# Kernel optimization log

Measured on AMD Instinct MI355X. Metric: run time of the kernel, lower is better.

The kernel has to match this reference:

```python
import jax, jax.numpy as jnp
import numpy as np

G, T, H, E, F, C = 8, 2048, 512, 8, 2048, 256


def setup_inputs() -> dict:
    key = jax.random.key(0)
    ks = jax.random.split(key, 4)
    s = 0.02  # truncated-normal stddev in the original init (plain normal here)
    return {
        "x": jax.random.normal(ks[0], (G, T, H), jnp.float32),
        "router_kernel": jax.random.normal(ks[1], (H, E), jnp.float32) * s,
        "router_bias": jnp.zeros((E,), jnp.float32),
        "wi": jax.random.normal(ks[2], (E, H, F), jnp.float32) * s,
        "bi": jnp.zeros((E, F), jnp.float32),
        "wo": jax.random.normal(ks[3], (E, F, H), jnp.float32) * s,
        "bo": jnp.zeros((E, H), jnp.float32),
        "expert_capacity": C,
    }


def reference(x, router_kernel, router_bias, wi, bi, wo, bo, expert_capacity):
    # ---- Router (eval mode: no jitter noise, no dropout) ----
    # logits / probs: [g, t, e]
    router_logits = jnp.einsum("gth,he->gte", x, router_kernel) + router_bias
    router_probs = jax.nn.softmax(router_logits, axis=-1)

    # Experts-choose masked routing: each expert picks its top-capacity tokens.
    probs_et = jnp.swapaxes(router_probs, 1, 2)              # [g, e, t]
    expert_gate, expert_index = jax.lax.top_k(probs_et, expert_capacity)  # [g, e, c]
    dispatch = jax.nn.one_hot(expert_index, x.shape[1], dtype=x.dtype)    # [g, e, c, t]
    combine = dispatch * expert_gate[..., None]                            # [g, e, c, t]

    # ---- Dispatch: gather tokens into per-expert buffers ----
    expert_inputs = jnp.einsum("gect,gth->gech", dispatch, x)  # [g, e, c, h]

    # ---- Per-expert FFN (batched einsum GEMMs) ----
    h_mid = jax.nn.gelu(
        jnp.einsum("gech,ehf->gecf", expert_inputs, wi) + bi[None, :, None, :],
        approximate=False,
    )
    expert_out = jnp.einsum("gecf,efh->gech", h_mid, wo) + bo[None, :, None, :]

    # ---- Combine: scatter expert outputs back, scaled by router prob ----
    y = jnp.einsum("gect,gech->gth", combine, expert_out)  # [g, t, h]
    return y
```

## Files before the change

### kernel.cpp

```cpp
#include <hip/hip_runtime.h>
#include <cstdint>
#include <cstddef>

#define G_ 8
#define T_ 2048
#define H_ 512
#define E_ 8
#define F_ 2048
#define C_ 256

typedef __bf16 bf16x8 __attribute__((ext_vector_type(8)));
typedef float f32x4 __attribute__((ext_vector_type(4)));

__device__ __forceinline__ unsigned short f2bf(float f) {
  unsigned u = __float_as_uint(f);
  u += 0x7FFFu + ((u >> 16) & 1u);
  return (unsigned short)(u >> 16);
}

__device__ __forceinline__ void gload_lds16(const void* g, void* l) {
  __builtin_amdgcn_global_load_lds(
      (const __attribute__((address_space(1))) void*)g,
      (__attribute__((address_space(3))) void*)l, 16, 0, 0);
}

__device__ __forceinline__ float fast_gelu(float v) {
  float z = v * (1.5957691216f + 0.0713540727f * v * v);
  float e = __expf(-z);
  return v * __builtin_amdgcn_rcpf(1.0f + e);
}

#define BARRIER() do { __builtin_amdgcn_s_barrier(); asm volatile("" ::: "memory"); } while (0)
#define WAIT_LDS() do { asm volatile("s_waitcnt lgkmcnt(0)" ::: "memory"); \
                        __builtin_amdgcn_sched_barrier(0); } while (0)

__device__ __forceinline__ void transconv_body(const float* __restrict__ in,
                                               unsigned short* __restrict__ out,
                                               int R, int Cc, int tC, int bidrem,
                                               float* smem) {
  int tid = threadIdx.x;
  int nT = (R / 64) * tC;
  int b = bidrem / nT;
  int rem = bidrem % nT;
  int tr = rem / tC, tc = rem % tC;
  const float* ib = in + (size_t)b * R * Cc + (size_t)(tr * 64) * Cc + tc * 64;
  unsigned short* ob = out + (size_t)b * R * Cc;
  int lr = tid >> 4, lc = (tid & 15) * 4;
#pragma unroll
  for (int i = 0; i < 4; ++i) {
    float4 v = *(const float4*)&ib[(size_t)(lr + 16 * i) * Cc + lc];
    smem[(lr + 16 * i) * 65 + lc + 0] = v.x;
    smem[(lr + 16 * i) * 65 + lc + 1] = v.y;
    smem[(lr + 16 * i) * 65 + lc + 2] = v.z;
    smem[(lr + 16 * i) * 65 + lc + 3] = v.w;
  }
  __syncthreads();
  int r = (tid & 31) * 2, c0 = tid >> 5;
#pragma unroll
  for (int i = 0; i < 8; ++i) {
    int c = c0 + i * 8;
    ushort2 o;
    o.x = f2bf(smem[r * 65 + c]);
    o.y = f2bf(smem[(r + 1) * 65 + c]);
    *(ushort2*)&ob[(size_t)(tc * 64 + c) * R + tr * 64 + r] = o;
  }
}

__device__ __forceinline__ void router_body(const float* __restrict__ x,
                                            const float* __restrict__ rk,
                                            const float* __restrict__ rb,
                                            float* __restrict__ probs,
                                            int bidrem, float* rks) {
  int tid = threadIdx.x;
  for (int i = tid; i < H_ * E_ / 4; i += 256)
    ((float4*)rks)[i] = ((const float4*)rk)[i];
  __syncthreads();
  int wid = tid >> 6, lane = tid & 63;
  int row = bidrem * 4 + wid;
  float acc[E_];
#pragma unroll
  for (int e = 0; e < E_; ++e) acc[e] = 0.f;
  const float* xr = x + (size_t)row * H_;
#pragma unroll
  for (int j = 0; j < H_ / 64; ++j) {
    int h = j * 64 + lane;
    float xv = xr[h];
    const float4* r4 = (const float4*)&rks[h * E_];
    float4 r0 = r4[0], r1 = r4[1];
    acc[0] += xv * r0.x; acc[1] += xv * r0.y; acc[2] += xv * r0.z; acc[3] += xv * r0.w;
    acc[4] += xv * r1.x; acc[5] += xv * r1.y; acc[6] += xv * r1.z; acc[7] += xv * r1.w;
  }
#pragma unroll
  for (int e = 0; e < E_; ++e) {
#pragma unroll
    for (int off = 32; off > 0; off >>= 1) acc[e] += __shfl_xor(acc[e], off);
  }
  float l[E_];
  float mx = -1e30f;
#pragma unroll
  for (int e = 0; e < E_; ++e) { l[e] = acc[e] + rb[e]; mx = fmaxf(mx, l[e]); }
  float s = 0.f;
#pragma unroll
  for (int e = 0; e < E_; ++e) { l[e] = expf(l[e] - mx); s += l[e]; }
  float inv = 1.0f / s;
  int g = row >> 11, t = row & (T_ - 1);
  if (lane < E_) probs[((size_t)(g * E_ + lane)) * T_ + t] = l[lane] * inv;
}

__global__ __launch_bounds__(256) void fused1_kernel(const float* __restrict__ wi,
                                                     unsigned short* __restrict__ wiT,
                                                     const float* __restrict__ wo,
                                                     unsigned short* __restrict__ woT,
                                                     const float* __restrict__ x,
                                                     const float* __restrict__ rk,
                                                     const float* __restrict__ rb,
                                                     float* __restrict__ probs) {
  __shared__ float smem[64 * 65];
  int bid = blockIdx.x;
  if (bid < 2048) {
    transconv_body(wi, wiT, H_, F_, F_ / 64, bid, smem);
  } else if (bid < 4096) {
    transconv_body(wo, woT, F_, H_, H_ / 64, bid - 2048, smem);
  } else {
    router_body(x, rk, rb, probs, bid - 4096, smem);
  }
}

__global__ __launch_bounds__(1024) void topk_kernel(const float* __restrict__ probs,
                                                    int* __restrict__ idx,
                                                    float* __restrict__ gate) {
  __shared__ unsigned long long keys[T_];
  int ge = blockIdx.x, tid = threadIdx.x;
  const float* p = probs + (size_t)ge * T_;
#pragma unroll
  for (int j = 0; j < 2; ++j) {
    int t = tid + j * 1024;
    unsigned pb = __float_as_uint(p[t]);
    keys[t] = ((unsigned long long)pb << 32) | (unsigned)(~t);
  }
  __syncthreads();
  for (unsigned k = 2; k <= T_; k <<= 1) {
    for (unsigned j = k >> 1; j > 0; j >>= 1) {
      unsigned w = tid;
      unsigned i = ((w & ~(j - 1)) << 1) | (w & (j - 1));
      unsigned q = i + j;
      unsigned long long a = keys[i], b = keys[q];
      bool sw = ((i & k) == 0) ? (a < b) : (a > b);
      if (sw) { keys[i] = b; keys[q] = a; }
      __syncthreads();
    }
  }
  if (tid < C_) {
    unsigned long long kk = keys[tid];
    gate[ge * C_ + tid] = __uint_as_float((unsigned)(kk >> 32));
    idx[ge * C_ + tid] = (int)(~(unsigned)kk);
  }
}

__global__ __launch_bounds__(256) void fused2_kernel(const float* __restrict__ x,
                                                     const int* __restrict__ idx,
                                                     unsigned short* __restrict__ xin,
                                                     int* __restrict__ cnt,
                                                     unsigned short* __restrict__ ent) {
  int bid = blockIdx.x, tid = threadIdx.x;
  if (bid < 4096) {
    int wid = tid >> 6, lane = tid & 63;
    int r = bid * 4 + wid;
    int ge = r >> 8;
    int g = ge >> 3;
    int t = idx[r];
    const float* src = x + ((size_t)(g * T_ + t)) * H_;
    unsigned short* dst = xin + (size_t)r * H_;
#pragma unroll
    for (int j = 0; j < 2; ++j) {
      int h = j * 256 + lane * 4;
      float4 v = *(const float4*)&src[h];
      ushort4 o;
      o.x = f2bf(v.x); o.y = f2bf(v.y); o.z = f2bf(v.z); o.w = f2bf(v.w);
      *(ushort4*)&dst[h] = o;
    }
  } else {
    int id = (bid - 4096) * 256 + tid;
    int ge = id >> 8, c = id & 255;
    int g = ge >> 3, e = ge & 7;
    int t = idx[id];
    int pos = atomicAdd(&cnt[g * T_ + t], 1);
    ent[(g * T_ + t) * 8 + pos] = (unsigned short)((e << 8) | c);
  }
}

__global__ __launch_bounds__(256) void combine_kernel(const unsigned short* __restrict__ eout,
                                                      const int* __restrict__ cnt,
                                                      const unsigned short* __restrict__ ent,
                                                      const float* __restrict__ gate,
                                                      float* __restrict__ y) {
  int tid = threadIdx.x, wid = tid >> 6, lane = tid & 63;
  int row = blockIdx.x * 4 + wid;
  int g = row >> 11;
  int n = cnt[row];
  float a[8] = {0.f, 0.f, 0.f, 0.f, 0.f, 0.f, 0.f, 0.f};
  for (int i = 0; i < n; ++i) {
    unsigned pe = ent[row * 8 + i];
    int e = pe >> 8, c = pe & 255;
    int ge = g * E_ + e;
    float gv = gate[ge * C_ + c];
    bf16x8 v = *(const bf16x8*)&eout[((size_t)ge * C_ + c) * H_ + lane * 8];
#pragma unroll
    for (int j = 0; j < 8; ++j) a[j] += gv * (float)v[j];
  }
  float* yr = y + (size_t)row * H_ + lane * 8;
  *(float4*)yr = make_float4(a[0], a[1], a[2], a[3]);
  *(float4*)(yr + 4) = make_float4(a[4], a[5], a[6], a[7]);
}

template<int NT>
__device__ __forceinline__ void gemm_core(const unsigned short* __restrict__ Abase,
                                          const unsigned short* __restrict__ Bbase,
                                          int ldK, unsigned short* lds,
                                          f32x4 (&acc)[8][4]) {
  int tid = threadIdx.x;
  int wid = tid >> 6, lane = tid & 63;
  int l15 = lane & 15, g4 = lane >> 4;
  int wm = wid >> 2, wn = wid & 3;

  int off0, off1;
  {
    int ob = tid * 16;
    int lr = ob >> 7, b = ((ob >> 4) & 7) ^ (lr & 7);
    off0 = (2 * lr + (b >> 2)) * ldK + (b & 3) * 8;
    ob = 8192 + tid * 16;
    lr = ob >> 7; b = ((ob >> 4) & 7) ^ (lr & 7);
    off1 = (2 * lr + (b >> 2)) * ldK + (b & 3) * 8;
  }
  int blkphys = (((l15 & 1) << 2) | g4) ^ (l15 >> 1);
  int abase = (wm * 64 + (l15 >> 1)) * 64 + blkphys * 8;
  int bbase = 8192 + (wn * 32 + (l15 >> 1)) * 64 + blkphys * 8;

  auto stageA = [&](int kt) {
    unsigned short* sb = lds + (kt & 3) * 16384;
    const unsigned short* ga = Abase + kt * 32;
    gload_lds16(ga + off0, sb + wid * 512);
    gload_lds16(ga + off1, sb + 4096 + wid * 512);
  };
  auto stageB = [&](int kt) {
    unsigned short* sb = lds + (kt & 3) * 16384;
    const unsigned short* gb = Bbase + kt * 32;
    gload_lds16(gb + off0, sb + 8192 + wid * 512);
    gload_lds16(gb + off1, sb + 12288 + wid * 512);
  };

  bf16x8 bfr[4];
  auto step = [&](int kt, int prefetch, int vmN) {
    const unsigned short* sb = lds + (kt & 3) * 16384;
    bf16x8 af[4];
#pragma unroll
    for (int m = 0; m < 4; ++m) af[m] = *(const bf16x8*)&sb[abase + m * 512];
#pragma unroll
    for (int n = 0; n < 4; ++n) bfr[n] = *(const bf16x8*)&sb[bbase + n * 512];
    if (prefetch) stageA(kt + 3);
    BARRIER();
    WAIT_LDS();
    __builtin_amdgcn_s_setprio(1);
#pragma unroll
    for (int m = 0; m < 4; ++m)
#pragma unroll
      for (int n = 0; n < 4; ++n)
        acc[m][n] = __builtin_amdgcn_mfma_f32_16x16x32_bf16(af[m], bfr[n], acc[m][n], 0, 0, 0);
    __builtin_amdgcn_s_setprio(0);
    BARRIER();
#pragma unroll
    for (int m = 0; m < 4; ++m) af[m] = *(const bf16x8*)&sb[abase + (4 + m) * 512];
    if (prefetch) stageB(kt + 3);
    if (vmN == 8) asm volatile("s_waitcnt vmcnt(8)" ::: "memory");
    else if (vmN == 4) asm volatile("s_waitcnt vmcnt(4)" ::: "memory");
    else if (vmN == 0) asm volatile("s_waitcnt vmcnt(0)" ::: "memory");
    BARRIER();
    WAIT_LDS();
    __builtin_amdgcn_s_setprio(1);
#pragma unroll
    for (int m = 0; m < 4; ++m)
#pragma unroll
      for (int n = 0; n < 4; ++n)
        acc[4 + m][n] = __builtin_amdgcn_mfma_f32_16x16x32_bf16(af[m], bfr[n], acc[4 + m][n], 0, 0, 0);
    __builtin_amdgcn_s_setprio(0);
    BARRIER();
  };

  stageA(0); stageB(0); stageA(1); stageB(1); stageA(2); stageB(2);
  asm volatile("s_waitcnt vmcnt(8)" ::: "memory");
  BARRIER();
  for (int kt = 0; kt < NT - 3; ++kt) step(kt, 1, 8);
  step(NT - 3, 0, 4);
  step(NT - 2, 0, 0);
  step(NT - 1, 0, -1);
}

__global__ __launch_bounds__(512, 2) void gemm1_kernel(const unsigned short* __restrict__ xin,
                                                       const unsigned short* __restrict__ wiT,
                                                       const float* __restrict__ bi,
                                                       unsigned short* __restrict__ hmid) {
  __shared__ unsigned short lds[65536];
  int bid = blockIdx.x;
  int swz = (bid & 7) * 64 + (bid >> 3);
  int e = swz >> 6, rem = swz & 63, nt = rem >> 3, g = rem & 7;
  int ge = g * E_ + e;
  const unsigned short* Abase = xin + (size_t)ge * C_ * H_;
  const unsigned short* Bbase = wiT + (size_t)e * F_ * H_ + (size_t)(nt * 256) * H_;
  f32x4 acc[8][4] = {};
  gemm_core<H_ / 32>(Abase, Bbase, H_, lds, acc);

  int tid = threadIdx.x, wid = tid >> 6, lane = tid & 63;
  int l15 = lane & 15, g4 = lane >> 4, wm = wid >> 2, wn = wid & 3;
  unsigned short* Cb = hmid + (size_t)ge * C_ * F_;
  int row0 = wm * 128, col0 = nt * 256 + wn * 64;
#pragma unroll
  for (int m = 0; m < 8; ++m) {
#pragma unroll
    for (int n = 0; n < 4; ++n) {
      int col = col0 + n * 16 + l15;
      float bv = bi[e * F_ + col];
#pragma unroll
      for (int r = 0; r < 4; ++r) {
        int row = row0 + m * 16 + g4 * 4 + r;
        Cb[(size_t)row * F_ + col] = f2bf(fast_gelu(acc[m][n][r] + bv));
      }
    }
  }
}

template<int NT>
__device__ __forceinline__ void gemm2_core(const unsigned short* __restrict__ Abase,
                                           const unsigned short* __restrict__ Bbase,
                                           int ldK, unsigned short* lds,
                                           f32x4 (&acc)[8][4]) {
  int tid = threadIdx.x;
  int wid = tid >> 6, lane = tid & 63;
  int l15 = lane & 15, g4 = lane >> 4;
  int wn = wid;

  auto mkoff = [&](int ob) {
    int lr = ob >> 7, b = ((ob >> 4) & 7) ^ (lr & 7);
    return (2 * lr + (b >> 2)) * ldK + (b & 3) * 8;
  };
  int offA0 = mkoff(tid * 16), offA1 = mkoff(4096 + tid * 16);
  int offB0 = mkoff(tid * 16), offB1 = mkoff(4096 + tid * 16);
  int offB2 = mkoff(8192 + tid * 16), offB3 = mkoff(12288 + tid * 16);

  int blkphys = (((l15 & 1) << 2) | g4) ^ (l15 >> 1);
  int abase = (l15 >> 1) * 64 + blkphys * 8;
  int bbase = 4096 + (wn * 32 + (l15 >> 1)) * 64 + blkphys * 8;

  auto stageA = [&](int kt, int slot) {
    unsigned short* sb = lds + slot * 12288;
    const unsigned short* ga = Abase + kt * 32;
    const unsigned short* gb = Bbase + kt * 32;
    gload_lds16(ga + offA0, sb + wid * 512);
    gload_lds16(ga + offA1, sb + 2048 + wid * 512);
    gload_lds16(gb + offB0, sb + 4096 + wid * 512);
  };
  auto stageB = [&](int kt, int slot) {
    unsigned short* sb = lds + slot * 12288;
    const unsigned short* gb = Bbase + kt * 32;
    gload_lds16(gb + offB1, sb + 6144 + wid * 512);
    gload_lds16(gb + offB2, sb + 8192 + wid * 512);
    gload_lds16(gb + offB3, sb + 10240 + wid * 512);
  };

  bf16x8 bfr[4];
  int s0 = 0, s1 = 1, s2 = 2;
  auto step = [&](int kt, int prefetch, int vmN) {
    const unsigned short* sb = lds + s0 * 12288;
    bf16x8 af[4];
#pragma unroll
    for (int m = 0; m < 4; ++m) af[m] = *(const bf16x8*)&sb[abase + m * 512];
#pragma unroll
    for (int n = 0; n < 4; ++n) bfr[n] = *(const bf16x8*)&sb[bbase + n * 512];
    if (prefetch) stageA(kt + 2, s2);
    BARRIER();
    WAIT_LDS();
    __builtin_amdgcn_s_setprio(1);
#pragma unroll
    for (int m = 0; m < 4; ++m)
#pragma unroll
      for (int n = 0; n < 4; ++n)
        acc[m][n] = __builtin_amdgcn_mfma_f32_16x16x32_bf16(af[m], bfr[n], acc[m][n], 0, 0, 0);
    __builtin_amdgcn_s_setprio(0);
    BARRIER();
#pragma unroll
    for (int m = 0; m < 4; ++m) af[m] = *(const bf16x8*)&sb[abase + (4 + m) * 512];
    if (prefetch) stageB(kt + 2, s2);
    if (vmN == 6) asm volatile("s_waitcnt vmcnt(6)" ::: "memory");
    else if (vmN == 0) asm volatile("s_waitcnt vmcnt(0)" ::: "memory");
    BARRIER();
    WAIT_LDS();
    __builtin_amdgcn_s_setprio(1);
#pragma unroll
    for (int m = 0; m < 4; ++m)
#pragma unroll
      for (int n = 0; n < 4; ++n)
        acc[4 + m][n] = __builtin_amdgcn_mfma_f32_16x16x32_bf16(af[m], bfr[n], acc[4 + m][n], 0, 0, 0);
    __builtin_amdgcn_s_setprio(0);
    BARRIER();
    int t = s0; s0 = s1; s1 = s2; s2 = t;
  };

  stageA(0, 0); stageB(0, 0); stageA(1, 1); stageB(1, 1);
  asm volatile("s_waitcnt vmcnt(6)" ::: "memory");
  BARRIER();
  for (int kt = 0; kt < NT - 2; ++kt) step(kt, 1, 6);
  step(NT - 2, 0, 0);
  step(NT - 1, 0, -1);
}

__global__ __launch_bounds__(256, 2) void gemm2_kernel(const unsigned short* __restrict__ hmid,
                                                       const unsigned short* __restrict__ woT,
                                                       const float* __restrict__ bo,
                                                       unsigned short* __restrict__ eout) {
  __shared__ unsigned short lds[36864];
  int bid = blockIdx.x;
  int swz = (bid & 7) * 32 + (bid >> 3);
  int e = swz >> 5, rem = swz & 31;
  int tile = rem >> 3, g = rem & 7;
  int tm = tile >> 1, tn = tile & 1;
  int ge = g * E_ + e;
  const unsigned short* Abase = hmid + (size_t)ge * C_ * F_ + (size_t)(tm * 128) * F_;
  const unsigned short* Bbase = woT + (size_t)e * H_ * F_ + (size_t)(tn * 256) * F_;
  f32x4 acc[8][4] = {};
  gemm2_core<F_ / 32>(Abase, Bbase, F_, lds, acc);

  int tid = threadIdx.x, wid = tid >> 6, lane = tid & 63;
  int l15 = lane & 15, g4 = lane >> 4, wn = wid;
  unsigned short* Ob = eout + (size_t)ge * C_ * H_;
  int row0 = tm * 128, col0 = tn * 256 + wn * 64;
#pragma unroll
  for (int m = 0; m < 8; ++m) {
#pragma unroll
    for (int n = 0; n < 4; ++n) {
      int col = col0 + n * 16 + l15;
      float bv = bo[e * H_ + col];
#pragma unroll
      for (int r = 0; r < 4; ++r) {
        int row = row0 + m * 16 + g4 * 4 + r;
        Ob[(size_t)row * H_ + col] = f2bf(acc[m][n][r] + bv);
      }
    }
  }
}

extern "C" void kernel_launch(void* const* d_in, const int* in_sizes, int n_in,
                              void* d_out, int out_size, void* d_ws, size_t ws_size,
                              hipStream_t stream) {
  const float* x  = (const float*)d_in[0];
  const float* rk = (const float*)d_in[1];
  const float* rb = (const float*)d_in[2];
  const float* wi = (const float*)d_in[3];
  const float* bi = (const float*)d_in[4];
  const float* wo = (const float*)d_in[5];
  const float* bo = (const float*)d_in[6];
  float* y = (float*)d_out;

  const size_t WI_T = 0;
  const size_t WO_T = 16777216;
  const size_t PROB = 33554432;
  const size_t IDXO = 34078720;
  const size_t GATO = 34144256;
  const size_t XINO = 34209792;
  const size_t HMID = 50987008;
  const size_t NEED = 118095872;
  if (ws_size < NEED) return;

  char* ws = (char*)d_ws;
  unsigned short* wiT = (unsigned short*)(ws + WI_T);
  unsigned short* woT = (unsigned short*)(ws + WO_T);
  float* probs = (float*)(ws + PROB);
  int* cnt = (int*)(ws + PROB);
  unsigned short* ent = (unsigned short*)(ws + PROB + 65536);
  int* idx = (int*)(ws + IDXO);
  float* gate = (float*)(ws + GATO);
  unsigned short* xin = (unsigned short*)(ws + XINO);
  unsigned short* eout = (unsigned short*)(ws + XINO);
  unsigned short* hmid = (unsigned short*)(ws + HMID);

  fused1_kernel<<<8192, 256, 0, stream>>>(wi, wiT, wo, woT, x, rk, rb, probs);
  topk_kernel<<<G_ * E_, 1024, 0, stream>>>(probs, idx, gate);
  hipMemsetAsync(cnt, 0, G_ * T_ * sizeof(int), stream);
  fused2_kernel<<<4096 + 64, 256, 0, stream>>>(x, idx, xin, cnt, ent);
  gemm1_kernel<<<512, 512, 0, stream>>>(xin, wiT, bi, hmid);
  gemm2_kernel<<<256, 256, 0, stream>>>(hmid, woT, bo, eout);
  combine_kernel<<<G_ * T_ / 4, 256, 0, stream>>>(eout, cnt, ent, gate, y);
}
```

Before: 161.1 us.

## Simplify GEMM k-loop pipelines and retile gemm2 to 128x128 blocks

The gemm1 main loop changes from split half-steps with four barriers per k-tile to a single stage-then-compute step. Each k-tile now prefetches A and B together three tiles ahead and waits once with vmcnt. gemm2 moves from 128x256 tiles with 256 blocks to 128x128 tiles with 512 blocks, arranged as 2x2 waves over a 4-slot LDS ring, which gives better CU coverage on a 256-CU part and lowers LDS use. The trade-off is less intra-step overlap between LDS reads and MFMA, plus more register pressure in gemm1 from holding 8 A fragments at once.

```diff
diff --git a/kernel.cpp b/kernel.cpp
--- a/kernel.cpp
+++ b/kernel.cpp
@@ -31,8 +31,6 @@
 }
 
 #define BARRIER() do { __builtin_amdgcn_s_barrier(); asm volatile("" ::: "memory"); } while (0)
-#define WAIT_LDS() do { asm volatile("s_waitcnt lgkmcnt(0)" ::: "memory"); \
-                        __builtin_amdgcn_sched_barrier(0); } while (0)
 
 __device__ __forceinline__ void transconv_body(const float* __restrict__ in,
                                                unsigned short* __restrict__ out,
@@ -236,63 +234,48 @@
   int abase = (wm * 64 + (l15 >> 1)) * 64 + blkphys * 8;
   int bbase = 8192 + (wn * 32 + (l15 >> 1)) * 64 + blkphys * 8;
 
-  auto stageA = [&](int kt) {
+  auto stage = [&](int kt) {
     unsigned short* sb = lds + (kt & 3) * 16384;
     const unsigned short* ga = Abase + kt * 32;
+    const unsigned short* gb = Bbase + kt * 32;
     gload_lds16(ga + off0, sb + wid * 512);
     gload_lds16(ga + off1, sb + 4096 + wid * 512);
-  };
-  auto stageB = [&](int kt) {
-    unsigned short* sb = lds + (kt & 3) * 16384;
-    const unsigned short* gb = Bbase + kt * 32;
     gload_lds16(gb + off0, sb + 8192 + wid * 512);
     gload_lds16(gb + off1, sb + 12288 + wid * 512);
   };
 
-  bf16x8 bfr[4];
-  auto step = [&](int kt, int prefetch, int vmN) {
+  auto compute = [&](int kt) {
     const unsigned short* sb = lds + (kt & 3) * 16384;
-    bf16x8 af[4];
-#pragma unroll
-    for (int m = 0; m < 4; ++m) af[m] = *(const bf16x8*)&sb[abase + m * 512];
+    bf16x8 af[8], bfr[4];
+#pragma unroll
+    for (int m = 0; m < 8; ++m) af[m] = *(const bf16x8*)&sb[abase + m * 512];
 #pragma unroll
     for (int n = 0; n < 4; ++n) bfr[n] = *(const bf16x8*)&sb[bbase + n * 512];
-    if (prefetch) stageA(kt + 3);
-    BARRIER();
-    WAIT_LDS();
     __builtin_amdgcn_s_setprio(1);
 #pragma unroll
-    for (int m = 0; m < 4; ++m)
+    for (int m = 0; m < 8; ++m)
 #pragma unroll
       for (int n = 0; n < 4; ++n)
         acc[m][n] = __builtin_amdgcn_mfma_f32_16x16x32_bf16(af[m], bfr[n], acc[m][n], 0, 0, 0);
     __builtin_amdgcn_s_setprio(0);
+  };
+
+  stage(0); stage(1); stage(2);
+  asm volatile("s_waitcnt vmcnt(8)" ::: "memory");
+  BARRIER();
+  for (int kt = 0; kt < NT - 3; ++kt) {
+    stage(kt + 3);
+    compute(kt);
+    asm volatile("s_waitcnt vmcnt(8)" ::: "memory");
     BARRIER();
-#pragma unroll
-    for (int m = 0; m < 4; ++m) af[m] = *(const bf16x8*)&sb[abase + (4 + m) * 512];
-    if (prefetch) stageB(kt + 3);
-    if (vmN == 8) asm volatile("s_waitcnt vmcnt(8)" ::: "memory");
-    else if (vmN == 4) asm volatile("s_waitcnt vmcnt(4)" ::: "memory");
-    else if (vmN == 0) asm volatile("s_waitcnt vmcnt(0)" ::: "memory");
-    BARRIER();
-    WAIT_LDS();
-    __builtin_amdgcn_s_setprio(1);
-#pragma unroll
-    for (int m = 0; m < 4; ++m)
-#pragma unroll
-      for (int n = 0; n < 4; ++n)
-        acc[4 + m][n] = __builtin_amdgcn_mfma_f32_16x16x32_bf16(af[m], bfr[n], acc[4 + m][n], 0, 0, 0);
-    __builtin_amdgcn_s_setprio(0);
-    BARRIER();
-  };
-
-  stageA(0); stageB(0); stageA(1); stageB(1); stageA(2); stageB(2);
-  asm volatile("s_waitcnt vmcnt(8)" ::: "memory");
-  BARRIER();
-  for (int kt = 0; kt < NT - 3; ++kt) step(kt, 1, 8);
-  step(NT - 3, 0, 4);
-  step(NT - 2, 0, 0);
-  step(NT - 1, 0, -1);
+  }
+  compute(NT - 3);
+  asm volatile("s_waitcnt vmcnt(4)" ::: "memory");
+  BARRIER();
+  compute(NT - 2);
+  asm volatile("s_waitcnt vmcnt(0)" ::: "memory");
+  BARRIER();
+  compute(NT - 1);
 }
 
 __global__ __launch_bounds__(512, 2) void gemm1_kernel(const unsigned short* __restrict__ xin,
@@ -332,52 +315,40 @@
 __device__ __forceinline__ void gemm2_core(const unsigned short* __restrict__ Abase,
                                            const unsigned short* __restrict__ Bbase,
                                            int ldK, unsigned short* lds,
-                                           f32x4 (&acc)[8][4]) {
+                                           f32x4 (&acc)[4][4]) {
   int tid = threadIdx.x;
   int wid = tid >> 6, lane = tid & 63;
   int l15 = lane & 15, g4 = lane >> 4;
-  int wn = wid;
+  int wm = wid >> 1, wn = wid & 1;
 
   auto mkoff = [&](int ob) {
     int lr = ob >> 7, b = ((ob >> 4) & 7) ^ (lr & 7);
     return (2 * lr + (b >> 2)) * ldK + (b & 3) * 8;
   };
-  int offA0 = mkoff(tid * 16), offA1 = mkoff(4096 + tid * 16);
-  int offB0 = mkoff(tid * 16), offB1 = mkoff(4096 + tid * 16);
-  int offB2 = mkoff(8192 + tid * 16), offB3 = mkoff(12288 + tid * 16);
+  int off0 = mkoff(tid * 16);
+  int off1 = mkoff(4096 + tid * 16);
 
   int blkphys = (((l15 & 1) << 2) | g4) ^ (l15 >> 1);
-  int abase = (l15 >> 1) * 64 + blkphys * 8;
+  int abase = (wm * 32 + (l15 >> 1)) * 64 + blkphys * 8;
   int bbase = 4096 + (wn * 32 + (l15 >> 1)) * 64 + blkphys * 8;
 
-  auto stageA = [&](int kt, int slot) {
-    unsigned short* sb = lds + slot * 12288;
+  auto stage = [&](int kt) {
+    unsigned short* sb = lds + (kt & 3) * 8192;
     const unsigned short* ga = Abase + kt * 32;
     const unsigned short* gb = Bbase + kt * 32;
-    gload_lds16(ga + offA0, sb + wid * 512);
-    gload_lds16(ga + offA1, sb + 2048 + wid * 512);
-    gload_lds16(gb + offB0, sb + 4096 + wid * 512);
+    gload_lds16(ga + off0, sb + wid * 512);
+    gload_lds16(ga + off1, sb + 2048 + wid * 512);
+    gload_lds16(gb + off0, sb + 4096 + wid * 512);
+    gload_lds16(gb + off1, sb + 6144 + wid * 512);
   };
-  auto stageB = [&](int kt, int slot) {
-    unsigned short* sb = lds + slot * 12288;
-    const unsigned short* gb = Bbase + kt * 32;
-    gload_lds16(gb + offB1, sb + 6144 + wid * 512);
-    gload_lds16(gb + offB2, sb + 8192 + wid * 512);
-    gload_lds16(gb + offB3, sb + 10240 + wid * 512);
-  };
-
-  bf16x8 bfr[4];
-  int s0 = 0, s1 = 1, s2 = 2;
-  auto step = [&](int kt, int prefetch, int vmN) {
-    const unsigned short* sb = lds + s0 * 12288;
-    bf16x8 af[4];
+
+  auto compute = [&](int kt) {
+    const unsigned short* sb = lds + (kt & 3) * 8192;
+    bf16x8 af[4], bfr[4];
 #pragma unroll
     for (int m = 0; m < 4; ++m) af[m] = *(const bf16x8*)&sb[abase + m * 512];
 #pragma unroll
     for (int n = 0; n < 4; ++n) bfr[n] = *(const bf16x8*)&sb[bbase + n * 512];
-    if (prefetch) stageA(kt + 2, s2);
-    BARRIER();
-    WAIT_LDS();
     __builtin_amdgcn_s_setprio(1);
 #pragma unroll
     for (int m = 0; m < 4; ++m)
@@ -385,55 +356,48 @@
       for (int n = 0; n < 4; ++n)
         acc[m][n] = __builtin_amdgcn_mfma_f32_16x16x32_bf16(af[m], bfr[n], acc[m][n], 0, 0, 0);
     __builtin_amdgcn_s_setprio(0);
+  };
+
+  stage(0); stage(1); stage(2);
+  asm volatile("s_waitcnt vmcnt(8)" ::: "memory");
+  BARRIER();
+  for (int kt = 0; kt < NT - 3; ++kt) {
+    stage(kt + 3);
+    compute(kt);
+    asm volatile("s_waitcnt vmcnt(8)" ::: "memory");
     BARRIER();
-#pragma unroll
-    for (int m = 0; m < 4; ++m) af[m] = *(const bf16x8*)&sb[abase + (4 + m) * 512];
-    if (prefetch) stageB(kt + 2, s2);
-    if (vmN == 6) asm volatile("s_waitcnt vmcnt(6)" ::: "memory");
-    else if (vmN == 0) asm volatile("s_waitcnt vmcnt(0)" ::: "memory");
-    BARRIER();
-    WAIT_LDS();
-    __builtin_amdgcn_s_setprio(1);
-#pragma unroll
-    for (int m = 0; m < 4; ++m)
-#pragma unroll
-      for (int n = 0; n < 4; ++n)
-        acc[4 + m][n] = __builtin_amdgcn_mfma_f32_16x16x32_bf16(af[m], bfr[n], acc[4 + m][n], 0, 0, 0);
-    __builtin_amdgcn_s_setprio(0);
-    BARRIER();
-    int t = s0; s0 = s1; s1 = s2; s2 = t;
-  };
-
-  stageA(0, 0); stageB(0, 0); stageA(1, 1); stageB(1, 1);
-  asm volatile("s_waitcnt vmcnt(6)" ::: "memory");
-  BARRIER();
-  for (int kt = 0; kt < NT - 2; ++kt) step(kt, 1, 6);
-  step(NT - 2, 0, 0);
-  step(NT - 1, 0, -1);
+  }
+  compute(NT - 3);
+  asm volatile("s_waitcnt vmcnt(4)" ::: "memory");
+  BARRIER();
+  compute(NT - 2);
+  asm volatile("s_waitcnt vmcnt(0)" ::: "memory");
+  BARRIER();
+  compute(NT - 1);
 }
 
 __global__ __launch_bounds__(256, 2) void gemm2_kernel(const unsigned short* __restrict__ hmid,
                                                        const unsigned short* __restrict__ woT,
                                                        const float* __restrict__ bo,
                                                        unsigned short* __restrict__ eout) {
-  __shared__ unsigned short lds[36864];
+  __shared__ unsigned short lds[32768];
   int bid = blockIdx.x;
-  int swz = (bid & 7) * 32 + (bid >> 3);
-  int e = swz >> 5, rem = swz & 31;
+  int swz = (bid & 7) * 64 + (bid >> 3);
+  int e = swz >> 6, rem = swz & 63;
   int tile = rem >> 3, g = rem & 7;
-  int tm = tile >> 1, tn = tile & 1;
+  int tm = tile >> 2, tn = tile & 3;
   int ge = g * E_ + e;
   const unsigned short* Abase = hmid + (size_t)ge * C_ * F_ + (size_t)(tm * 128) * F_;
-  const unsigned short* Bbase = woT + (size_t)e * H_ * F_ + (size_t)(tn * 256) * F_;
-  f32x4 acc[8][4] = {};
+  const unsigned short* Bbase = woT + (size_t)e * H_ * F_ + (size_t)(tn * 128) * F_;
+  f32x4 acc[4][4] = {};
   gemm2_core<F_ / 32>(Abase, Bbase, F_, lds, acc);
 
   int tid = threadIdx.x, wid = tid >> 6, lane = tid & 63;
-  int l15 = lane & 15, g4 = lane >> 4, wn = wid;
+  int l15 = lane & 15, g4 = lane >> 4, wm = wid >> 1, wn = wid & 1;
   unsigned short* Ob = eout + (size_t)ge * C_ * H_;
-  int row0 = tm * 128, col0 = tn * 256 + wn * 64;
-#pragma unroll
-  for (int m = 0; m < 8; ++m) {
+  int row0 = tm * 128 + wm * 64, col0 = tn * 128 + wn * 64;
+#pragma unroll
+  for (int m = 0; m < 4; ++m) {
 #pragma unroll
     for (int n = 0; n < 4; ++n) {
       int col = col0 + n * 16 + l15;
@@ -486,6 +450,6 @@
   hipMemsetAsync(cnt, 0, G_ * T_ * sizeof(int), stream);
   fused2_kernel<<<4096 + 64, 256, 0, stream>>>(x, idx, xin, cnt, ent);
   gemm1_kernel<<<512, 512, 0, stream>>>(xin, wiT, bi, hmid);
-  gemm2_kernel<<<256, 256, 0, stream>>>(hmid, woT, bo, eout);
+  gemm2_kernel<<<512, 256, 0, stream>>>(hmid, woT, bo, eout);
   combine_kernel<<<G_ * T_ / 4, 256, 0, stream>>>(eout, cnt, ent, gate, y);
 }
```

Result: slower. 164.5 us (+2.1%).
